# Kernel tuning notes

Measured on AMD Instinct MI355X. Metric: run time of the kernel, lower is better.

The kernel has to match this reference:

```python
import jax, jax.numpy as jnp
import numpy as np

N = 10           # node count hardcoded in original module
FEAT_IN = 3      # position(2) + orientation(1)
FEAT_OUT = 16    # 'simple' mode
FEAT_CC = 2 * FEAT_OUT
B = 16384
NEG_SLOPE = 0.2


def _pair_index():
    # Faithful pair ordering: for node i, row 0 is the self-pair (i,i),
    # rows 1..N-1 are j != i in ascending order.
    idx = np.empty((N, N), dtype=np.int32)
    for i in range(N):
        idx[i, 0] = i
        idx[i, 1:] = [j for j in range(N) if j != i]
    return jnp.asarray(idx)


def setup_inputs() -> dict:
    key = jax.random.key(0)
    ks = jax.random.split(key, 12)
    s = 0.1
    return {
        "position": jax.random.normal(ks[0], (B, N, 2), dtype=jnp.float32),
        "orientation": jax.random.normal(ks[1], (B, N, 1), dtype=jnp.float32),
        # preliminary_transform: Linear(3 -> 16)
        "Wp": jax.random.normal(ks[2], (FEAT_IN, FEAT_OUT), dtype=jnp.float32) * s,
        "bp": jax.random.normal(ks[3], (FEAT_OUT,), dtype=jnp.float32) * s,
        # connectivity_net: Linear(32->32), LReLU, Linear(32->8), LReLU, Linear(8->2)
        "W1": jax.random.normal(ks[4], (FEAT_CC, 32), dtype=jnp.float32) * s,
        "b1": jax.random.normal(ks[5], (32,), dtype=jnp.float32) * s,
        "W2": jax.random.normal(ks[6], (32, 8), dtype=jnp.float32) * s,
        "b2": jax.random.normal(ks[7], (8,), dtype=jnp.float32) * s,
        "W3": jax.random.normal(ks[8], (8, 2), dtype=jnp.float32) * s,
        "b3": jax.random.normal(ks[9], (2,), dtype=jnp.float32) * s,
    }


def reference(position, orientation, Wp, bp, W1, b1, W2, b2, W3, b3):
    lrelu = lambda x: jnp.where(x >= 0, x, NEG_SLOPE * x)
    # [B, N, 3] -> [B, N, 16]
    feat = jnp.concatenate([position, orientation], axis=2) @ Wp + bp
    idx = _pair_index()                                   # [N, N]
    vj = feat[:, idx]                                     # [B, N, N, 16] gathered partners
    vi = jnp.broadcast_to(feat[:, :, None, :], vj.shape)  # [B, N, N, 16] source node
    pair = jnp.concatenate([vi, vj], axis=-1)             # [B, N, N, 32]
    h = lrelu(pair @ W1 + b1)
    h = lrelu(h @ W2 + b2)
    big_edge = h @ W3 + b3                                # [B, N, N, 2]
    adjacency = jnp.argmax(big_edge, axis=3)              # [B, N, N]
    return big_edge, adjacency
```

## Files before the change

### kernel.cpp

```cpp
#include <hip/hip_runtime.h>


typedef float v2f __attribute__((ext_vector_type(2)));
typedef float v4f __attribute__((ext_vector_type(4)));

constexpr int G = 25;
constexpr int GB_STRIDE = 36;
constexpr float NEG = 0.2f;

__global__ __launch_bounds__(256, 4) void gpn_kernel(
    const float* __restrict__ pos,
    const float* __restrict__ ori,
    const float* __restrict__ Wp,
    const float* __restrict__ bp,
    const float* __restrict__ W1,
    const float* __restrict__ b1,
    const float* __restrict__ W2,
    const float* __restrict__ b2,
    const float* __restrict__ W3,
    const float* __restrict__ b3,
    float* __restrict__ out,
    int B)
{
    __shared__ float sM[3 * 64];
    __shared__ float sc[64];
    __shared__ float sgb[G * 10 * GB_STRIDE];

    const int t = threadIdx.x;
    const int bBase = blockIdx.x * G;
    const int remG = B - bBase;
    const int nNodes = ((remG < G) ? remG : G) * 10;

    {
        if (t < 192) {
            const int d = t >> 6, k = t & 63;
            const int kk = k & 31;
            const int fo = (k < 32) ? 0 : 16;
            float acc = 0.f;
#pragma unroll
            for (int f = 0; f < 16; ++f)
                acc = fmaf(Wp[d * 16 + f], W1[(fo + f) * 32 + kk], acc);
            sM[d * 64 + k] = acc;
        } else {
            const int k = t - 192;
            const int kk = k & 31;
            const int fo = (k < 32) ? 0 : 16;
            float acc = 0.f;
#pragma unroll
            for (int f = 0; f < 16; ++f)
                acc = fmaf(bp[f], W1[(fo + f) * 32 + kk], acc);
            if (k < 32) acc += b1[k];
            sc[k] = acc;
        }
    }
    __syncthreads();

    v4f ga[8];
    const int g = t / 10;
    const int i = t - g * 10;
    if (t < nNodes) {
        const int node = bBase * 10 + t;
        const v2f p = ((const v2f*)pos)[node];
        const float o = ori[node];
        const v4f* m4 = (const v4f*)sM;
        const v4f* c4 = (const v4f*)sc;
        v4f* dst = (v4f*)&sgb[t * GB_STRIDE];
#pragma unroll
        for (int q = 0; q < 16; ++q) {
            v4f gg = c4[q];
            gg += p.x * m4[q];
            gg += p.y * m4[16 + q];
            gg += o   * m4[32 + q];
            if (q < 8) ga[q] = gg;
            else       dst[q - 8] = gg;
        }
    }
    __syncthreads();

    if (t < nNodes) {
        const v2f* w2p = (const v2f*)W2;
        const v2f* w3p = (const v2f*)W3;
        const v2f bb2_0 = ((const v2f*)b2)[0];
        const v2f bb2_1 = ((const v2f*)b2)[1];
        const v2f bb2_2 = ((const v2f*)b2)[2];
        const v2f bb2_3 = ((const v2f*)b2)[3];
        const v2f bb3   = ((const v2f*)b3)[0];

        float evb[20];
        float adj[10];

#pragma unroll
        for (int c = 0; c < 10; ++c) {
            const int j = (c == 0) ? i : (((c - 1) < i) ? (c - 1) : c);
            const v4f* src = (const v4f*)&sgb[(g * 10 + j) * GB_STRIDE];

            v2f a0 = bb2_0, a1 = bb2_1, a2 = bb2_2, a3 = bb2_3;
#pragma unroll
            for (int q = 0; q < 8; ++q) {
                const v4f s = ga[q] + src[q];
                const v4f h = __builtin_elementwise_max(s, s * NEG);
                const int k0 = 4 * q;
                a0 += h.x * w2p[4 * (k0 + 0) + 0];
                a1 += h.x * w2p[4 * (k0 + 0) + 1];
                a2 += h.x * w2p[4 * (k0 + 0) + 2];
                a3 += h.x * w2p[4 * (k0 + 0) + 3];
                a0 += h.y * w2p[4 * (k0 + 1) + 0];
                a1 += h.y * w2p[4 * (k0 + 1) + 1];
                a2 += h.y * w2p[4 * (k0 + 1) + 2];
                a3 += h.y * w2p[4 * (k0 + 1) + 3];
                a0 += h.z * w2p[4 * (k0 + 2) + 0];
                a1 += h.z * w2p[4 * (k0 + 2) + 1];
                a2 += h.z * w2p[4 * (k0 + 2) + 2];
                a3 += h.z * w2p[4 * (k0 + 2) + 3];
                a0 += h.w * w2p[4 * (k0 + 3) + 0];
                a1 += h.w * w2p[4 * (k0 + 3) + 1];
                a2 += h.w * w2p[4 * (k0 + 3) + 2];
                a3 += h.w * w2p[4 * (k0 + 3) + 3];
            }

            const v2f h20 = __builtin_elementwise_max(a0, a0 * NEG);
            const v2f h21 = __builtin_elementwise_max(a1, a1 * NEG);
            const v2f h22 = __builtin_elementwise_max(a2, a2 * NEG);
            const v2f h23 = __builtin_elementwise_max(a3, a3 * NEG);

            v2f ev = bb3;
            ev += h20.x * w3p[0];
            ev += h20.y * w3p[1];
            ev += h21.x * w3p[2];
            ev += h21.y * w3p[3];
            ev += h22.x * w3p[4];
            ev += h22.y * w3p[5];
            ev += h23.x * w3p[6];
            ev += h23.y * w3p[7];

            evb[2 * c]     = ev.x;
            evb[2 * c + 1] = ev.y;
            adj[c] = (ev.y > ev.x) ? 1.0f : 0.0f;
        }

        const int eBase = (bBase * 10 + t) * 10;
        v4f* bo = (v4f*)(out + (size_t)eBase * 2);
#pragma unroll
        for (int q = 0; q < 5; ++q) {
            v4f vv = {evb[4 * q], evb[4 * q + 1], evb[4 * q + 2], evb[4 * q + 3]};
            bo[q] = vv;
        }
        v2f* ao = (v2f*)(out + (size_t)B * 200 + eBase);
#pragma unroll
        for (int q = 0; q < 5; ++q) {
            v2f vv = {adj[2 * q], adj[2 * q + 1]};
            ao[q] = vv;
        }
    }
}

extern "C" void kernel_launch(void* const* d_in, const int* in_sizes, int n_in,
                              void* d_out, int out_size, void* d_ws, size_t ws_size,
                              hipStream_t stream) {
    const float* pos = (const float*)d_in[0];
    const float* ori = (const float*)d_in[1];
    const float* Wp  = (const float*)d_in[2];
    const float* bp  = (const float*)d_in[3];
    const float* W1  = (const float*)d_in[4];
    const float* b1  = (const float*)d_in[5];
    const float* W2  = (const float*)d_in[6];
    const float* b2  = (const float*)d_in[7];
    const float* W3  = (const float*)d_in[8];
    const float* b3  = (const float*)d_in[9];
    float* out = (float*)d_out;

    const int B = in_sizes[0] / 20;
    const int nBlocks = (B + G - 1) / G;

    gpn_kernel<<<nBlocks, 256, 0, stream>>>(pos, ori, Wp, bp, W1, b1, W2, b2,
                                            W3, b3, out, B);
}
```

Baseline: 104.0 us.

## Split each node's ten edges across two threads and halve batch-per-block

Each node's 10 partner edges are now split between two adjacent threads (5 each), and each block covers 12 batch elements instead of 25, which more than doubles the block count. Both lanes compute the first half of the projected features, and each lane writes half of the partner-half features to shared memory. The aim is more parallelism and shorter per-thread serial chains, so latency is hidden better. In exchange, each thread's output stores shrink from vectorized 16-byte chunks to per-edge 8-byte and 4-byte stores, and the per-node feature computation is partly duplicated.

```diff
diff --git a/kernel.cpp b/kernel.cpp
--- a/kernel.cpp
+++ b/kernel.cpp
@@ -4,7 +4,7 @@
 typedef float v2f __attribute__((ext_vector_type(2)));
 typedef float v4f __attribute__((ext_vector_type(4)));
 
-constexpr int G = 25;
+constexpr int G = 12;
 constexpr int GB_STRIDE = 36;
 constexpr float NEG = 0.2f;
 
@@ -29,55 +29,63 @@
     const int t = threadIdx.x;
     const int bBase = blockIdx.x * G;
     const int remG = B - bBase;
-    const int nNodes = ((remG < G) ? remG : G) * 10;
+    const int nLanes = ((remG < G) ? remG : G) * 10 * 2;
 
-    {
-        if (t < 192) {
-            const int d = t >> 6, k = t & 63;
-            const int kk = k & 31;
-            const int fo = (k < 32) ? 0 : 16;
-            float acc = 0.f;
+    if (t < 192) {
+        const int d = t >> 6, k = t & 63;
+        const int kk = k & 31;
+        const int fo = (k < 32) ? 0 : 16;
+        float acc = 0.f;
 #pragma unroll
-            for (int f = 0; f < 16; ++f)
-                acc = fmaf(Wp[d * 16 + f], W1[(fo + f) * 32 + kk], acc);
-            sM[d * 64 + k] = acc;
-        } else {
-            const int k = t - 192;
-            const int kk = k & 31;
-            const int fo = (k < 32) ? 0 : 16;
-            float acc = 0.f;
+        for (int f = 0; f < 16; ++f)
+            acc = fmaf(Wp[d * 16 + f], W1[(fo + f) * 32 + kk], acc);
+        sM[d * 64 + k] = acc;
+    } else {
+        const int k = t - 192;
+        const int kk = k & 31;
+        const int fo = (k < 32) ? 0 : 16;
+        float acc = 0.f;
 #pragma unroll
-            for (int f = 0; f < 16; ++f)
-                acc = fmaf(bp[f], W1[(fo + f) * 32 + kk], acc);
-            if (k < 32) acc += b1[k];
-            sc[k] = acc;
+        for (int f = 0; f < 16; ++f)
+            acc = fmaf(bp[f], W1[(fo + f) * 32 + kk], acc);
+        if (k < 32) acc += b1[k];
+        sc[k] = acc;
+    }
+    __syncthreads();
+
+    v4f ga[8];
+    const int r = t >> 1;
+    const int half = t & 1;
+    const int g = r / 10;
+    const int i = r - g * 10;
+    if (t < nLanes) {
+        const int node = bBase * 10 + r;
+        const v2f p = ((const v2f*)pos)[node];
+        const float o = ori[node];
+        const v4f* m4 = (const v4f*)sM;
+        const v4f* c4 = (const v4f*)sc;
+        v4f* dst = (v4f*)&sgb[r * GB_STRIDE];
+#pragma unroll
+        for (int q = 0; q < 8; ++q) {
+            v4f gg = c4[q];
+            gg += p.x * m4[q];
+            gg += p.y * m4[16 + q];
+            gg += o   * m4[32 + q];
+            ga[q] = gg;
+        }
+#pragma unroll
+        for (int qq = 0; qq < 4; ++qq) {
+            const int q = 8 + half * 4 + qq;
+            v4f gg = c4[q];
+            gg += p.x * m4[q];
+            gg += p.y * m4[16 + q];
+            gg += o   * m4[32 + q];
+            dst[q - 8] = gg;
         }
     }
     __syncthreads();
 
-    v4f ga[8];
-    const int g = t / 10;
-    const int i = t - g * 10;
-    if (t < nNodes) {
-        const int node = bBase * 10 + t;
-        const v2f p = ((const v2f*)pos)[node];
-        const float o = ori[node];
-        const v4f* m4 = (const v4f*)sM;
-        const v4f* c4 = (const v4f*)sc;
-        v4f* dst = (v4f*)&sgb[t * GB_STRIDE];
-#pragma unroll
-        for (int q = 0; q < 16; ++q) {
-            v4f gg = c4[q];
-            gg += p.x * m4[q];
-            gg += p.y * m4[16 + q];
-            gg += o   * m4[32 + q];
-            if (q < 8) ga[q] = gg;
-            else       dst[q - 8] = gg;
-        }
-    }
-    __syncthreads();
-
-    if (t < nNodes) {
+    if (t < nLanes) {
         const v2f* w2p = (const v2f*)W2;
         const v2f* w3p = (const v2f*)W3;
         const v2f bb2_0 = ((const v2f*)b2)[0];
@@ -86,11 +94,12 @@
         const v2f bb2_3 = ((const v2f*)b2)[3];
         const v2f bb3   = ((const v2f*)b3)[0];
 
-        float evb[20];
-        float adj[10];
+        const int eRow = (bBase + g) * 100 + i * 10;
+        const size_t adjOff = (size_t)B * 200;
 
 #pragma unroll
-        for (int c = 0; c < 10; ++c) {
+        for (int cc = 0; cc < 5; ++cc) {
+            const int c = half * 5 + cc;
             const int j = (c == 0) ? i : (((c - 1) < i) ? (c - 1) : c);
             const v4f* src = (const v4f*)&sgb[(g * 10 + j) * GB_STRIDE];
 
@@ -133,23 +142,9 @@
             ev += h23.x * w3p[6];
             ev += h23.y * w3p[7];
 
-            evb[2 * c]     = ev.x;
-            evb[2 * c + 1] = ev.y;
-            adj[c] = (ev.y > ev.x) ? 1.0f : 0.0f;
-        }
-
-        const int eBase = (bBase * 10 + t) * 10;
-        v4f* bo = (v4f*)(out + (size_t)eBase * 2);
-#pragma unroll
-        for (int q = 0; q < 5; ++q) {
-            v4f vv = {evb[4 * q], evb[4 * q + 1], evb[4 * q + 2], evb[4 * q + 3]};
-            bo[q] = vv;
-        }
-        v2f* ao = (v2f*)(out + (size_t)B * 200 + eBase);
-#pragma unroll
-        for (int q = 0; q < 5; ++q) {
-            v2f vv = {adj[2 * q], adj[2 * q + 1]};
-            ao[q] = vv;
+            const int E = eRow + c;
+            ((v2f*)out)[E] = ev;
+            out[adjOff + E] = (ev.y > ev.x) ? 1.0f : 0.0f;
         }
     }
 }
```

Result: no change. 103.5 us (-0.4%).
